# Kernel optimization log

Measured on AMD Instinct MI355X. Metric: run time of the kernel, lower is better.

The kernel has to match this reference:

```python
import jax, jax.numpy as jnp
import numpy as np
import math

L = 2; B = 128; CIN = 64; E = 64; H = 8; Wd = 8; NH = 8; MEM = 40
HD = E // NH; HW = H * Wd; THD = HD * HW  # 512
MASK_B = 3.0; NEG = -1e9; EPS = 1e-5


def _conv(x, w, b):
    y = jax.lax.conv_general_dilated(x, w, (1, 1), 'SAME',
                                     dimension_numbers=('NCHW', 'OIHW', 'NCHW'))
    return y + b[None, :, None, None]


def setup_inputs() -> dict:
    key = jax.random.key(0)
    ks = jax.random.split(key, 12)
    f = jax.random.normal
    return {
        'x': f(ks[0], (B, CIN, H, Wd), jnp.float32),
        'h0': f(ks[1], (L, B, E, H, Wd), jnp.float32),
        'c0': f(ks[2], (L, B, E, H, Wd), jnp.float32),
        'k0': f(ks[3], (L, B, NH, MEM, THD), jnp.float32),
        'v0': f(ks[4], (L, B, NH, MEM, THD), jnp.float32),
        'src_mask': jax.random.randint(ks[5], (B, MEM), 0, 2).astype(bool),
        'notdone': jnp.ones((B,), bool),
        'main_w': f(ks[6], (L, 5 * E, CIN + 2 * E, 3, 3), jnp.float32) * 0.05,
        'main_b': jnp.zeros((L, 5 * E), jnp.float32),
        'proj_w': f(ks[7], (L, 3 * E, CIN + E, 3, 3), jnp.float32) * 0.05,
        'proj_b': jnp.zeros((L, 3 * E), jnp.float32),
        'out_w': f(ks[8], (L, E, E, 3, 3), jnp.float32) * 0.05,
        'out_b': jnp.zeros((L, E), jnp.float32),
        'ln_w': jnp.ones((L, E, H, Wd), jnp.float32),
        'ln_b': jnp.zeros((L, E, H, Wd), jnp.float32),
        'pos_w': f(ks[9], (L, MEM, HW * E), jnp.float32) * 0.05,
        'pos_b': f(ks[10], (L, MEM, NH), jnp.float32) * 0.05,
    }


def reference(x, h0, c0, k0, v0, src_mask, notdone,
              main_w, main_b, proj_w, proj_b, out_w, out_b,
              ln_w, ln_b, pos_w, pos_b):
    nd = notdone.astype(x.dtype)[:, None, None, None]
    # rolling attention mask: reset finished episodes, shift left, open last slot
    m = src_mask | (~notdone)[:, None]
    m = jnp.concatenate([m[:, 1:], jnp.zeros((B, 1), bool)], axis=1)
    bias = jnp.where(m, NEG, 0.0).astype(x.dtype)        # (B, MEM)
    bias = bias.at[:, -1].set(MASK_B)
    out = h0[L - 1] * nd
    for n in range(L):
        inp = jnp.concatenate([x, out], axis=1)          # (B, CIN+E, H, W)
        h_cur = h0[n] * nd
        c_cur = c0[n] * nd
        gates = _conv(jnp.concatenate([inp, h_cur], axis=1), main_w[n], main_b[n])
        cc_i, cc_f, cc_o, cc_g, cc_a = jnp.split(gates, 5, axis=1)
        i = jax.nn.sigmoid(cc_i)
        fg = jax.nn.sigmoid(cc_f)
        o = jax.nn.sigmoid(cc_o)
        g = jnp.tanh(cc_g)
        a = jax.nn.sigmoid(cc_a)
        c_next = fg * c_cur + i * g
        # attention over rolling memory (mem_n slots of flattened spatial features)
        kqv = _conv(inp, proj_w[n], proj_b[n]).reshape(B, NH, 3 * HD, HW)
        k = kqv[:, :, :HD].reshape(B, NH, THD)
        q = kqv[:, :, HD:2 * HD].reshape(B, NH, THD) / math.sqrt(THD)
        v = kqv[:, :, 2 * HD:].reshape(B, NH, THD)
        pw = pos_w[n].reshape(MEM, NH, THD).transpose(1, 0, 2)  # (NH, MEM, THD)
        k_cat = jnp.concatenate([k0[n][:, :, 1:], k[:, :, None, :]], axis=2) + pw[None]
        v_cat = jnp.concatenate([v0[n][:, :, 1:], v[:, :, None, :]], axis=2)
        scores = (jnp.einsum('bnd,bnmd->bnm', q, k_cat)
                  + bias[:, None, :] + pos_b[n].T[None])
        attn_w = jax.nn.softmax(scores, axis=-1)
        attn = jnp.einsum('bnm,bnmd->bnd', attn_w, v_cat).reshape(B, E, H, Wd)
        ao = _conv(attn, out_w[n], out_b[n]) + inp[:, :E]
        mu = ao.mean(axis=(1, 2, 3), keepdims=True)
        var = ((ao - mu) ** 2).mean(axis=(1, 2, 3), keepdims=True)
        ao = (ao - mu) * jax.lax.rsqrt(var + EPS) * ln_w[n][None] + ln_b[n][None]
        c_next = c_next + a * jnp.tanh(ao)
        out = o * jnp.tanh(c_next)
    return out
```

## Files before the change

### kernel.cpp

```cpp
#include <hip/hip_runtime.h>
#include <hip/hip_bf16.h>

typedef __hip_bfloat16 bf16;
typedef unsigned short u16;
typedef __attribute__((ext_vector_type(8))) short short8;
typedef __attribute__((ext_vector_type(4))) float f32x4;

#define Bb   128
#define MEMm 40

__device__ __forceinline__ float LD(const void* p, size_t i, int f32) {
    return f32 ? ((const float*)p)[i] : __bfloat162float(((const bf16*)p)[i]);
}
__device__ __forceinline__ float S2F(short s) {
    u16 u = (u16)s;
    return __bfloat162float(*(bf16*)&u);
}
__device__ __forceinline__ int LDB(const void* p, int i, int isbyte) {
    return isbyte ? (int)((const unsigned char*)p)[i] : ((const int*)p)[i];
}
__device__ __forceinline__ void SPLIT(float v, u16& hi, u16& lo) {
    bf16 h = __float2bfloat16(v);
    float r = v - __bfloat162float(h);
    bf16 l = __float2bfloat16(r);
    hi = *(u16*)&h; lo = *(u16*)&l;
}

__global__ void setup_kernel(const void* __restrict__ x,
                             const void* __restrict__ src_mask,
                             const void* __restrict__ notdone,
                             const void* __restrict__ h0,
                             const void* __restrict__ mw,
                             const void* __restrict__ pw,
                             const void* __restrict__ ow,
                             int* __restrict__ flags,
                             float* __restrict__ biasb,
                             float* __restrict__ outb, size_t hoff,
                             u16* __restrict__ whi, u16* __restrict__ wlo) {
    __shared__ int det[3];
    const int bid = blockIdx.x, t = threadIdx.x;
    if (t < 3) det[t] = 0;
    __syncthreads();
    {
        const bf16* xb = (const bf16*)x;
        int bad = 0;
        for (int i = t; i < 4096; i += 256) {
            float v = __bfloat162float(xb[2 * i]);
            if (!(fabsf(v) < 1e4f)) bad = 1;
        }
        if (bad) atomicOr(&det[0], 1);
        int mb = 0;
        const unsigned* mi = (const unsigned*)src_mask;
        for (int i = t; i < 1280; i += 256) if (mi[i] > 1u) mb = 1;
        if (mb) atomicOr(&det[1], 1);
        int nb = 0;
        const unsigned* ni = (const unsigned*)notdone;
        for (int i = t; i < 32; i += 256) if (ni[i] > 1u) nb = 1;
        if (nb) atomicOr(&det[2], 1);
    }
    __syncthreads();
    const int isf32 = det[0], mbyte = det[1], ndbyte = det[2];
    if (bid == 0 && t < 3) flags[t] = det[t];

    if (bid < 20) {
        int idx = bid * 256 + t;
        if (idx >= Bb * MEMm) return;
        int b = idx / MEMm, m = idx - b * MEMm;
        float v;
        if (m == MEMm - 1) v = 3.0f;
        else {
            bool masked = (LDB(src_mask, b * MEMm + m + 1, mbyte) != 0) ||
                          (LDB(notdone, b, ndbyte) == 0);
            v = masked ? -1e9f : 0.f;
        }
        biasb[idx] = v;
    } else if (bid < 276) {
        int idx = (bid - 20) * 256 + t;
        int b = idx >> 9;
        float nd = (LDB(notdone, b, ndbyte) != 0) ? 1.f : 0.f;
        size_t e = (size_t)idx * 8;
        float v[8];
        if (isf32) {
            const float* hp = (const float*)h0 + hoff + e;
            f32x4 p0 = *(const f32x4*)hp, p1 = *(const f32x4*)(hp + 4);
#pragma unroll
            for (int j = 0; j < 4; ++j) { v[j] = p0[j]; v[4 + j] = p1[j]; }
        } else {
            short8 s = *(const short8*)((const bf16*)h0 + hoff + e);
#pragma unroll
            for (int j = 0; j < 8; ++j) v[j] = S2F(s[j]);
        }
#pragma unroll
        for (int j = 0; j < 8; ++j) outb[e + j] = v[j] * nd;
    } else {
        int gi = (bid - 276) * 256 + t;
        if (gi >= 1622016) return;
        int layer = (gi >= 811008) ? 1 : 0;
        int i = gi - layer * 811008;
        float v;
        if (i < 552960) {
            int tap = i / 61440, r = i - tap * 61440, co = r / 192, ci = r - co * 192;
            v = LD(mw, (size_t)layer * 552960 + ((size_t)co * 192 + ci) * 9 + tap, isf32);
        } else if (i < 774144) {
            int j = i - 552960;
            int tap = j / 24576, r = j - tap * 24576, co = r / 128, ci = r - co * 128;
            v = LD(pw, (size_t)layer * 221184 + ((size_t)co * 128 + ci) * 9 + tap, isf32);
        } else {
            int j = i - 774144;
            int tap = j / 4096, r = j - tap * 4096, co = r / 64, ci = r - co * 64;
            v = LD(ow, (size_t)layer * 36864 + ((size_t)co * 64 + ci) * 9 + tap, isf32);
        }
        u16 h, l; SPLIT(v, h, l);
        whi[gi] = h; wlo[gi] = l;
    }
}

struct ConvArgs {
    const void *x; const float *prev_out; const void *h0; const void *notdone;
    const u16 *WhiA, *WloA, *WhiB, *WloB;
    const void *biasA, *biasB;
    float *OutA, *OutB;
    long long boffA, boffB;
    size_t hoff;
    int KciA, KciB, CoutA, CoutB, ntA, NT, NMB;
};

__global__ __launch_bounds__(256) void conv_mfma_kernel(ConvArgs g,
                                                        const int* __restrict__ flags) {
    __shared__ __align__(16) u16 Alds[2][2][2600];
    __shared__ __align__(16) u16 Wlds[2][2][2560];
    const int t = threadIdx.x, w = t >> 6, lane = t & 63;
    const int bpair = w >> 1, half = w & 1;
    const int bx = blockIdx.x;
    const int mblk = bx % g.NMB, nt = bx / g.NMB;
    const bool isA = (nt < g.ntA);
    const u16* Whi = isA ? g.WhiA : g.WhiB;
    const u16* Wlo = isA ? g.WloA : g.WloB;
    const int Kci  = isA ? g.KciA : g.KciB;
    const int CoutT= isA ? g.CoutA : g.CoutB;
    float* Out     = isA ? g.OutA : g.OutB;
    const void* bias = isA ? g.biasA : g.biasB;
    const long long boff = isA ? g.boffA : g.boffB;
    const int n0 = (isA ? nt : nt - g.ntA) * 64;
    const int b = mblk * 2 + bpair;
    const int NITER = (Kci >> 5) * 9;
    const int isf32 = flags[0];
    const float nd = (LDB(g.notdone, b, flags[2]) != 0) ? 1.f : 0.f;

    if (half == 0 && lane < 40) { Alds[bpair][0][2560 + lane] = 0; Alds[bpair][1][2560 + lane] = 0; }

    f32x4 acc[4][2];
#pragma unroll
    for (int i = 0; i < 4; ++i)
#pragma unroll
        for (int j = 0; j < 2; ++j) { f32x4 z = {0.f, 0.f, 0.f, 0.f}; acc[i][j] = z; }

    const int co_l = t >> 2, jj = t & 3;
    uint4 hvA, lvA, hvB, lvB;
    auto issueW = [&](int it, uint4& hv, uint4& lv) {
        int kc = it / 9, tap = it - kc * 9;
        size_t o = ((size_t)(tap * CoutT + n0 + co_l)) * Kci + kc * 32 + jj * 8;
        hv = *(const uint4*)(Whi + o);
        lv = *(const uint4*)(Wlo + o);
    };

    issueW(0, hvA, lvA);
    issueW(1, hvB, lvB);
    for (int it = 0; it < NITER; ++it) {
        const int kc = it / 9, tap = it - kc * 9;
        const int par = it & 1;
        *(uint4*)&Wlds[par][0][co_l * 40 + jj * 8] = hvA;
        *(uint4*)&Wlds[par][1][co_l * 40 + jj * 8] = lvA;
        __syncthreads();
        hvA = hvB; lvA = lvB;
        if (it + 2 < NITER) issueW(it + 2, hvB, lvB);
        if (tap == 0) {
            const int px = lane;
            const int c0i = half * 16;
            const int cbase = kc * 32;
            short8 hA, hB, lA, lB;
#pragma unroll
            for (int cl2 = 0; cl2 < 16; ++cl2) {
                int c = cbase + c0i + cl2;
                float v;
                if (c < 64) {
                    size_t o = (size_t)b * 4096 + (size_t)c * 64 + px;
                    v = isf32 ? ((const float*)g.x)[o] : S2F(((const short*)g.x)[o]);
                } else if (c < 128) {
                    v = g.prev_out[(size_t)b * 4096 + (size_t)(c - 64) * 64 + px];
                } else {
                    size_t o = g.hoff + (size_t)b * 4096 + (size_t)(c - 128) * 64 + px;
                    v = (isf32 ? ((const float*)g.h0)[o] : S2F(((const short*)g.h0)[o])) * nd;
                }
                u16 hh, ll; SPLIT(v, hh, ll);
                if (cl2 < 8) { hA[cl2] = (short)hh; lA[cl2] = (short)ll; }
                else         { hB[cl2 - 8] = (short)hh; lB[cl2 - 8] = (short)ll; }
            }
            *(short8*)&Alds[bpair][0][px * 40 + c0i]     = hA;
            *(short8*)&Alds[bpair][0][px * 40 + c0i + 8] = hB;
            *(short8*)&Alds[bpair][1][px * 40 + c0i]     = lA;
            *(short8*)&Alds[bpair][1][px * 40 + c0i + 8] = lB;
            __syncthreads();
        }
        const int dy = tap / 3 - 1, dx = tap % 3 - 1;
        const int q8 = (lane >> 4) * 8;
        const int ml = lane & 15;
        short8 aH[4], aL[4];
#pragma unroll
        for (int mt = 0; mt < 4; ++mt) {
            int px = mt * 16 + ml;
            int yy = (px >> 3) + dy, xx = (px & 7) + dx;
            int row = ((unsigned)yy < 8u && (unsigned)xx < 8u) ? yy * 8 + xx : 64;
            int o = row * 40 + q8;
            aH[mt] = *(const short8*)&Alds[bpair][0][o];
            aL[mt] = *(const short8*)&Alds[bpair][1][o];
        }
#pragma unroll
        for (int nn = 0; nn < 2; ++nn) {
            int o = (half * 32 + nn * 16 + ml) * 40 + q8;
            short8 bH = *(const short8*)&Wlds[par][0][o];
            short8 bL = *(const short8*)&Wlds[par][1][o];
#pragma unroll
            for (int mt = 0; mt < 4; ++mt) {
                acc[mt][nn] = __builtin_amdgcn_mfma_f32_16x16x32_bf16(aH[mt], bH, acc[mt][nn], 0, 0, 0);
                acc[mt][nn] = __builtin_amdgcn_mfma_f32_16x16x32_bf16(aH[mt], bL, acc[mt][nn], 0, 0, 0);
                acc[mt][nn] = __builtin_amdgcn_mfma_f32_16x16x32_bf16(aL[mt], bH, acc[mt][nn], 0, 0, 0);
            }
        }
    }
    const int q = lane >> 4, ml = lane & 15;
#pragma unroll
    for (int nn = 0; nn < 2; ++nn) {
        int co = n0 + half * 32 + nn * 16 + ml;
        float bv = LD(bias, (size_t)boff + co, isf32);
#pragma unroll
        for (int mt = 0; mt < 4; ++mt) {
            f32x4 v = acc[mt][nn];
            v[0] += bv; v[1] += bv; v[2] += bv; v[3] += bv;
            *(f32x4*)&Out[((size_t)b * CoutT + co) * 64 + mt * 16 + q * 4] = v;
        }
    }
}

__global__ __launch_bounds__(256) void attn_kernel(
    const float* __restrict__ kqv,
    const void* __restrict__ k0,
    const void* __restrict__ v0,
    const void* __restrict__ pw,
    const void* __restrict__ pb,
    const float* __restrict__ biasb,
    const int* __restrict__ flags,
    u16* __restrict__ ahi, u16* __restrict__ alo,
    size_t kvoff, size_t pwoff, size_t pboff) {
    __shared__ float qv[512], kl[512], vl[512], sc[40], wexp[40];
    __shared__ float accbuf[4][512];
    const int t = threadIdx.x;
    const int isf32 = flags[0];
    const int b = blockIdx.x >> 3, h = blockIdx.x & 7;
    const size_t kqb = (size_t)b * 192 * 64;
    for (int d = t; d < 512; d += 256) {
        int hd = d >> 6, ss = d & 63;
        qv[d] = kqv[kqb + (h * 24 + 8 + hd) * 64 + ss] * 0.044194173824159216f;
        kl[d] = kqv[kqb + (h * 24 + 0 + hd) * 64 + ss];
        vl[d] = kqv[kqb + (h * 24 + 16 + hd) * 64 + ss];
    }
    __syncthreads();
    const int wid = t >> 6, lane = t & 63;
    const int d0 = lane * 8;
    const size_t kvbase = kvoff + ((size_t)(b * 8 + h)) * (size_t)(40 * 512);

    float q8[8];
#pragma unroll
    for (int j = 0; j < 8; ++j) q8[j] = qv[d0 + j];

    if (!isf32) {
        const bf16* kp = (const bf16*)k0;
        const bf16* pp = (const bf16*)pw;
        const bf16* vp = (const bf16*)v0;
        short8 kr[10], pr[10];
#pragma unroll
        for (int i = 0; i < 10; ++i) {
            int m = wid + i * 4;
            pr[i] = *(const short8*)(pp + pwoff + (size_t)m * 4096 + h * 512 + d0);
            if (m < 39)
                kr[i] = *(const short8*)(kp + kvbase + (size_t)(m + 1) * 512 + d0);
        }
#pragma unroll
        for (int i = 0; i < 10; ++i) {
            int m = wid + i * 4;
            float p = 0.f;
            if (m < 39) {
#pragma unroll
                for (int j = 0; j < 8; ++j)
                    p += q8[j] * (S2F(kr[i][j]) + S2F(pr[i][j]));
            } else {
#pragma unroll
                for (int j = 0; j < 8; ++j)
                    p += q8[j] * (kl[d0 + j] + S2F(pr[i][j]));
            }
#pragma unroll
            for (int off = 32; off > 0; off >>= 1) p += __shfl_down(p, off, 64);
            if (lane == 0)
                sc[m] = p + biasb[b * 40 + m] + LD(pb, pboff + m * 8 + h, 0);
        }
        short8 vr[10];
#pragma unroll
        for (int i = 0; i < 10; ++i) {
            int m = wid + i * 4;
            if (m < 39)
                vr[i] = *(const short8*)(vp + kvbase + (size_t)(m + 1) * 512 + d0);
        }
        __syncthreads();
        float mx = -1e30f;
        for (int m = 0; m < 40; ++m) mx = fmaxf(mx, sc[m]);
        if (t < 40) wexp[t] = __expf(sc[t] - mx);
        __syncthreads();
        float sum = 0.f;
        for (int m = 0; m < 40; ++m) sum += wexp[m];
        float rs = 1.f / sum;
        float acc8[8];
#pragma unroll
        for (int j = 0; j < 8; ++j) acc8[j] = 0.f;
#pragma unroll
        for (int i = 0; i < 10; ++i) {
            int m = wid + i * 4;
            float wgt = wexp[m];
            if (m < 39) {
#pragma unroll
                for (int j = 0; j < 8; ++j) acc8[j] += wgt * S2F(vr[i][j]);
            } else {
#pragma unroll
                for (int j = 0; j < 8; ++j) acc8[j] += wgt * vl[d0 + j];
            }
        }
#pragma unroll
        for (int j = 0; j < 8; ++j) accbuf[wid][d0 + j] = acc8[j];
        __syncthreads();
        for (int d = t; d < 512; d += 256) {
            float acc = (accbuf[0][d] + accbuf[1][d]) + (accbuf[2][d] + accbuf[3][d]);
            acc *= rs;
            int ch = h * 8 + (d >> 6), px = d & 63;
            u16 hh, ll; SPLIT(acc, hh, ll);
            size_t o = (size_t)b * 4096 + px * 64 + ch;
            ahi[o] = hh; alo[o] = ll;
        }
        return;
    }

    for (int m = wid; m < 40; m += 4) {
        float kc[8];
        if (m < 39) {
            const float* kp = (const float*)k0 + kvbase + (size_t)(m + 1) * 512 + d0;
            f32x4 p0 = *(const f32x4*)kp, p1 = *(const f32x4*)(kp + 4);
#pragma unroll
            for (int j = 0; j < 4; ++j) { kc[j] = p0[j]; kc[4 + j] = p1[j]; }
        } else {
#pragma unroll
            for (int j = 0; j < 8; ++j) kc[j] = kl[d0 + j];
        }
        const float* pp = (const float*)pw + pwoff + (size_t)m * 4096 + h * 512 + d0;
        f32x4 p0 = *(const f32x4*)pp, p1 = *(const f32x4*)(pp + 4);
#pragma unroll
        for (int j = 0; j < 4; ++j) { kc[j] += p0[j]; kc[4 + j] += p1[j]; }
        float p = 0.f;
#pragma unroll
        for (int j = 0; j < 8; ++j) p += q8[j] * kc[j];
#pragma unroll
        for (int off = 32; off > 0; off >>= 1) p += __shfl_down(p, off, 64);
        if (lane == 0)
            sc[m] = p + biasb[b * 40 + m] + LD(pb, pboff + m * 8 + h, 1);
    }
    __syncthreads();
    float mx = -1e30f;
    for (int m = 0; m < 40; ++m) mx = fmaxf(mx, sc[m]);
    if (t < 40) wexp[t] = __expf(sc[t] - mx);
    __syncthreads();
    float sum = 0.f;
    for (int m = 0; m < 40; ++m) sum += wexp[m];
    float rs = 1.f / sum;
    float acc8[8];
#pragma unroll
    for (int j = 0; j < 8; ++j) acc8[j] = 0.f;
    for (int m = wid; m < 40; m += 4) {
        float wgt = wexp[m];
        if (m < 39) {
            const float* vp = (const float*)v0 + kvbase + (size_t)(m + 1) * 512 + d0;
            f32x4 p0 = *(const f32x4*)vp, p1 = *(const f32x4*)(vp + 4);
#pragma unroll
            for (int j = 0; j < 4; ++j) { acc8[j] += wgt * p0[j]; acc8[4 + j] += wgt * p1[j]; }
        } else {
#pragma unroll
            for (int j = 0; j < 8; ++j) acc8[j] += wgt * vl[d0 + j];
        }
    }
#pragma unroll
    for (int j = 0; j < 8; ++j) accbuf[wid][d0 + j] = acc8[j];
    __syncthreads();
    for (int d = t; d < 512; d += 256) {
        float acc = (accbuf[0][d] + accbuf[1][d]) + (accbuf[2][d] + accbuf[3][d]);
        acc *= rs;
        int ch = h * 8 + (d >> 6), px = d & 63;
        u16 hh, ll; SPLIT(acc, hh, ll);
        size_t o = (size_t)b * 4096 + px * 64 + ch;
        ahi[o] = hh; alo[o] = ll;
    }
}

__global__ __launch_bounds__(256) void tail_kernel(
    const u16* __restrict__ ahi, const u16* __restrict__ alo,
    const u16* __restrict__ whi, const u16* __restrict__ wlo,
    const void* __restrict__ outb_bias,
    const void* __restrict__ x,
    const float* __restrict__ gates,
    const void* __restrict__ c0,
    const void* __restrict__ notdone,
    const void* __restrict__ lnw, const void* __restrict__ lnb,
    const int* __restrict__ flags,
    float* __restrict__ out_buf, void* __restrict__ dout, int write_out,
    long long boff, size_t coff, size_t lnoff) {
    __shared__ __align__(16) u16 Ald[2][2][2600];
    __shared__ __align__(16) u16 Wl[2][2][2560];
    __shared__ float red[8], stats[2];
    const int t = threadIdx.x, w = t >> 6, lane = t & 63;
    const int b = blockIdx.x;
    const int isf32 = flags[0], ndbyte = flags[2];

    {
        int px = t >> 2, ci16 = (t & 3) * 16;
        int chunk = ci16 >> 5, cl = ci16 & 31;
        size_t o = ((size_t)b * 64 + px) * 64 + ci16;
        *(uint4*)&Ald[chunk][0][px * 40 + cl]     = *(const uint4*)(ahi + o);
        *(uint4*)&Ald[chunk][0][px * 40 + cl + 8] = *(const uint4*)(ahi + o + 8);
        *(uint4*)&Ald[chunk][1][px * 40 + cl]     = *(const uint4*)(alo + o);
        *(uint4*)&Ald[chunk][1][px * 40 + cl + 8] = *(const uint4*)(alo + o + 8);
        if (t < 160) { int ch = t / 80, hl = (t / 40) & 1, i = t % 40;
                       Ald[ch][hl][2560 + i] = 0; }
    }

    const int co_l = t >> 2, jj = t & 3;
    uint4 hv, lv;
    auto issueW = [&](int it) {
        int kc = it / 9, tap = it - kc * 9;
        size_t o = ((size_t)(tap * 64 + co_l)) * 64 + kc * 32 + jj * 8;
        hv = *(const uint4*)(whi + o);
        lv = *(const uint4*)(wlo + o);
    };

    f32x4 acc[4];
#pragma unroll
    for (int i = 0; i < 4; ++i) { f32x4 z = {0.f, 0.f, 0.f, 0.f}; acc[i] = z; }

    issueW(0);
    for (int it = 0; it < 18; ++it) {
        const int kc = it / 9, tap = it - kc * 9;
        const int par = it & 1;
        *(uint4*)&Wl[par][0][co_l * 40 + jj * 8] = hv;
        *(uint4*)&Wl[par][1][co_l * 40 + jj * 8] = lv;
        __syncthreads();
        if (it + 1 < 18) issueW(it + 1);
        const int dy = tap / 3 - 1, dx = tap % 3 - 1;
        const int q8 = (lane >> 4) * 8;
        const int ml = lane & 15;
        short8 aH[4], aL[4];
#pragma unroll
        for (int mt = 0; mt < 4; ++mt) {
            int px = mt * 16 + ml;
            int yy = (px >> 3) + dy, xx = (px & 7) + dx;
            int row = ((unsigned)yy < 8u && (unsigned)xx < 8u) ? yy * 8 + xx : 64;
            int o = row * 40 + q8;
            aH[mt] = *(const short8*)&Ald[kc][0][o];
            aL[mt] = *(const short8*)&Ald[kc][1][o];
        }
        int o = (w * 16 + ml) * 40 + q8;
        short8 bH = *(const short8*)&Wl[par][0][o];
        short8 bL = *(const short8*)&Wl[par][1][o];
#pragma unroll
        for (int mt = 0; mt < 4; ++mt) {
            acc[mt] = __builtin_amdgcn_mfma_f32_16x16x32_bf16(aH[mt], bH, acc[mt], 0, 0, 0);
            acc[mt] = __builtin_amdgcn_mfma_f32_16x16x32_bf16(aH[mt], bL, acc[mt], 0, 0, 0);
            acc[mt] = __builtin_amdgcn_mfma_f32_16x16x32_bf16(aL[mt], bH, acc[mt], 0, 0, 0);
        }
    }

    const int q = lane >> 4, ml = lane & 15;
    const int co = w * 16 + ml;
    const size_t base = (size_t)b * 4096;
    float bv = LD(outb_bias, (size_t)boff + co, isf32);
    float vals[16];
    float sum = 0.f, sumsq = 0.f;
#pragma unroll
    for (int mt = 0; mt < 4; ++mt) {
        int px0 = mt * 16 + q * 4;
#pragma unroll
        for (int r = 0; r < 4; ++r) {
            float xv = LD(x, base + (size_t)co * 64 + px0 + r, isf32);
            float val = acc[mt][r] + bv + xv;
            vals[mt * 4 + r] = val; sum += val; sumsq += val * val;
        }
    }
#pragma unroll
    for (int off = 32; off > 0; off >>= 1) {
        sum   += __shfl_down(sum, off, 64);
        sumsq += __shfl_down(sumsq, off, 64);
    }
    if (lane == 0) { red[w] = sum; red[4 + w] = sumsq; }
    __syncthreads();
    if (t == 0) {
        float ts = red[0] + red[1] + red[2] + red[3];
        float tq = red[4] + red[5] + red[6] + red[7];
        float mu = ts * (1.f / 4096.f);
        float var = tq * (1.f / 4096.f) - mu * mu;
        stats[0] = mu; stats[1] = rsqrtf(fmaxf(var, 0.f) + 1e-5f);
    }
    __syncthreads();
    const float mu = stats[0], rstd = stats[1];
    const float nd = (LDB(notdone, b, ndbyte) != 0) ? 1.f : 0.f;
    const size_t gbase = (size_t)b * 320 * 64;
#pragma unroll
    for (int mt = 0; mt < 4; ++mt) {
        int px0 = mt * 16 + q * 4;
        size_t i0 = (size_t)co * 64 + px0;
        f32x4 gi4 = *(const f32x4*)&gates[gbase + (size_t)(co      ) * 64 + px0];
        f32x4 gf4 = *(const f32x4*)&gates[gbase + (size_t)(co +  64) * 64 + px0];
        f32x4 go4 = *(const f32x4*)&gates[gbase + (size_t)(co + 128) * 64 + px0];
        f32x4 gg4 = *(const f32x4*)&gates[gbase + (size_t)(co + 192) * 64 + px0];
        f32x4 ga4 = *(const f32x4*)&gates[gbase + (size_t)(co + 256) * 64 + px0];
        f32x4 ov;
#pragma unroll
        for (int r = 0; r < 4; ++r) {
            size_t i = i0 + r;
            float aon = (vals[mt * 4 + r] - mu) * rstd * LD(lnw, lnoff + i, isf32)
                        + LD(lnb, lnoff + i, isf32);
            float gi = 1.f / (1.f + __expf(-gi4[r]));
            float gf = 1.f / (1.f + __expf(-gf4[r]));
            float go = 1.f / (1.f + __expf(-go4[r]));
            float gg = tanhf(gg4[r]);
            float ga = 1.f / (1.f + __expf(-ga4[r]));
            float cc = LD(c0, coff + base + i, isf32) * nd;
            float cn = gf * cc + gi * gg + ga * tanhf(aon);
            float o  = go * tanhf(cn);
            ov[r] = o;
            if (write_out) {
                if (isf32) ((float*)dout)[base + i] = o;
                else       ((bf16*)dout)[base + i] = __float2bfloat16(o);
            }
        }
        *(f32x4*)&out_buf[base + i0] = ov;
    }
}

extern "C" void kernel_launch(void* const* d_in, const int* in_sizes, int n_in,
                              void* d_out, int out_size, void* d_ws, size_t ws_size,
                              hipStream_t stream) {
    const void* x      = d_in[0];
    const void* h0     = d_in[1];
    const void* c0     = d_in[2];
    const void* k0     = d_in[3];
    const void* v0     = d_in[4];
    const void* src_mask = d_in[5];
    const void* notdone  = d_in[6];
    const void* main_w = d_in[7];
    const void* main_b = d_in[8];
    const void* proj_w = d_in[9];
    const void* proj_b = d_in[10];
    const void* out_w  = d_in[11];
    const void* out_b  = d_in[12];
    const void* ln_w   = d_in[13];
    const void* ln_b   = d_in[14];
    const void* pos_w  = d_in[15];
    const void* pos_b  = d_in[16];

    float* wsf = (float*)d_ws;
    int*   flags    = (int*)d_ws;
    float* bias_buf = wsf + 8;
    float* out_buf  = wsf + 8192;
    float* gates_buf= wsf + 532480;
    float* kqv_buf  = wsf + 3153920;
    u16* attn_hi    = (u16*)(wsf + 4726784);
    u16* attn_lo    = (u16*)(wsf + 4988928);
    u16* wr_hi      = (u16*)(wsf + 5251072);
    u16* wr_lo      = (u16*)(wsf + 6062080);

    setup_kernel<<<6612, 256, 0, stream>>>(x, src_mask, notdone, h0,
                                           main_w, proj_w, out_w, flags,
                                           bias_buf, out_buf, (size_t)524288,
                                           wr_hi, wr_lo);
    for (int n = 0; n < 2; ++n) {
        const size_t wb = (size_t)n * 811008;
        ConvArgs ga;
        ga.x = x; ga.prev_out = out_buf; ga.h0 = h0; ga.notdone = notdone;
        ga.hoff = (size_t)n * 524288;
        ga.WhiA = wr_hi + wb;          ga.WloA = wr_lo + wb;          ga.KciA = 192; ga.CoutA = 320;
        ga.WhiB = wr_hi + wb + 552960; ga.WloB = wr_lo + wb + 552960; ga.KciB = 128; ga.CoutB = 192;
        ga.biasA = main_b; ga.boffA = (long long)n * 320; ga.OutA = gates_buf;
        ga.biasB = proj_b; ga.boffB = (long long)n * 192; ga.OutB = kqv_buf;
        ga.ntA = 5; ga.NT = 8; ga.NMB = 64;
        conv_mfma_kernel<<<512, 256, 0, stream>>>(ga, flags);

        attn_kernel<<<1024, 256, 0, stream>>>(
            kqv_buf, k0, v0, pos_w, pos_b, bias_buf, flags, attn_hi, attn_lo,
            (size_t)n * 20971520, (size_t)n * 163840, (size_t)n * 320);

        tail_kernel<<<128, 256, 0, stream>>>(
            attn_hi, attn_lo, wr_hi + wb + 774144, wr_lo + wb + 774144,
            out_b, x, gates_buf, c0, notdone, ln_w, ln_b, flags,
            out_buf, d_out, (n == 1) ? 1 : 0,
            (long long)n * 64, (size_t)n * 524288, (size_t)n * 4096);
    }
}
```

Before: 580.0 us.

## Pre-swizzle conv weights into MFMA fragment layout and load directly to registers

The weight-prep kernel now writes main and projection conv weights in a layout where each 512-element block matches one wave's 16x32 MFMA B-fragment, ordered by tap, k-chunk and output slice. The conv kernel drops the shared-memory weight staging buffer and its per-iteration barrier, and loads B fragments straight from global memory into registers with one-iteration prefetch. This removes LDS traffic and a __syncthreads per K step. In exchange each wave issues its own global loads, with only a single step of latency hiding. The out-projection layout is unchanged, so any path that reuses this conv kernel for it would read wrongly indexed weights.

```diff
diff --git a/kernel.cpp b/kernel.cpp
--- a/kernel.cpp
+++ b/kernel.cpp
@@ -99,15 +99,27 @@
         int i = gi - layer * 811008;
         float v;
         if (i < 552960) {
-            int tap = i / 61440, r = i - tap * 61440, co = r / 192, ci = r - co * 192;
+            int blk = i >> 9, r = i & 511;
+            int l = r >> 3, j = r & 7;
+            int nn = blk & 1, b2 = blk >> 1;
+            int s = b2 % 10, tk = b2 / 10;
+            int kc = tk % 6, tap = tk / 6;
+            int co = s * 32 + nn * 16 + (l & 15);
+            int ci = kc * 32 + ((l >> 4) << 3) + j;
             v = LD(mw, (size_t)layer * 552960 + ((size_t)co * 192 + ci) * 9 + tap, isf32);
         } else if (i < 774144) {
-            int j = i - 552960;
-            int tap = j / 24576, r = j - tap * 24576, co = r / 128, ci = r - co * 128;
+            int j2 = i - 552960;
+            int blk = j2 >> 9, r = j2 & 511;
+            int l = r >> 3, j = r & 7;
+            int nn = blk & 1, b2 = blk >> 1;
+            int s = b2 % 6, tk = b2 / 6;
+            int kc = tk & 3, tap = tk >> 2;
+            int co = s * 32 + nn * 16 + (l & 15);
+            int ci = kc * 32 + ((l >> 4) << 3) + j;
             v = LD(pw, (size_t)layer * 221184 + ((size_t)co * 128 + ci) * 9 + tap, isf32);
         } else {
-            int j = i - 774144;
-            int tap = j / 4096, r = j - tap * 4096, co = r / 64, ci = r - co * 64;
+            int j2 = i - 774144;
+            int tap = j2 / 4096, r = j2 - tap * 4096, co = r / 64, ci = r - co * 64;
             v = LD(ow, (size_t)layer * 36864 + ((size_t)co * 64 + ci) * 9 + tap, isf32);
         }
         u16 h, l; SPLIT(v, h, l);
@@ -128,7 +140,6 @@
 __global__ __launch_bounds__(256) void conv_mfma_kernel(ConvArgs g,
                                                         const int* __restrict__ flags) {
     __shared__ __align__(16) u16 Alds[2][2][2600];
-    __shared__ __align__(16) u16 Wlds[2][2][2560];
     const int t = threadIdx.x, w = t >> 6, lane = t & 63;
     const int bpair = w >> 1, half = w & 1;
     const int bx = blockIdx.x;
@@ -143,7 +154,10 @@
     const long long boff = isA ? g.boffA : g.boffB;
     const int n0 = (isA ? nt : nt - g.ntA) * 64;
     const int b = mblk * 2 + bpair;
-    const int NITER = (Kci >> 5) * 9;
+    const int kcN = Kci >> 5;
+    const int CoutT32 = CoutT >> 5;
+    const int NITER = kcN * 9;
+    const int s = (n0 >> 5) + half;
     const int isf32 = flags[0];
     const float nd = (LDB(g.notdone, b, flags[2]) != 0) ? 1.f : 0.f;
 
@@ -155,26 +169,28 @@
 #pragma unroll
         for (int j = 0; j < 2; ++j) { f32x4 z = {0.f, 0.f, 0.f, 0.f}; acc[i][j] = z; }
 
-    const int co_l = t >> 2, jj = t & 3;
-    uint4 hvA, lvA, hvB, lvB;
-    auto issueW = [&](int it, uint4& hv, uint4& lv) {
+    auto wbase = [&](int it) -> size_t {
         int kc = it / 9, tap = it - kc * 9;
-        size_t o = ((size_t)(tap * CoutT + n0 + co_l)) * Kci + kc * 32 + jj * 8;
-        hv = *(const uint4*)(Whi + o);
-        lv = *(const uint4*)(Wlo + o);
+        return ((size_t)((tap * kcN + kc) * CoutT32 + s) * 2) * 512 + (size_t)lane * 8;
     };
 
-    issueW(0, hvA, lvA);
-    issueW(1, hvB, lvB);
+    short8 wh0, wh1, wl0, wl1, nh0, nh1, nl0, nl1;
+    {
+        size_t o = wbase(0);
+        wh0 = *(const short8*)(Whi + o); wh1 = *(const short8*)(Whi + o + 512);
+        wl0 = *(const short8*)(Wlo + o); wl1 = *(const short8*)(Wlo + o + 512);
+    }
+    nh0 = wh0; nh1 = wh1; nl0 = wl0; nl1 = wl1;
+
     for (int it = 0; it < NITER; ++it) {
         const int kc = it / 9, tap = it - kc * 9;
-        const int par = it & 1;
-        *(uint4*)&Wlds[par][0][co_l * 40 + jj * 8] = hvA;
-        *(uint4*)&Wlds[par][1][co_l * 40 + jj * 8] = lvA;
-        __syncthreads();
-        hvA = hvB; lvA = lvB;
-        if (it + 2 < NITER) issueW(it + 2, hvB, lvB);
+        if (it + 1 < NITER) {
+            size_t o = wbase(it + 1);
+            nh0 = *(const short8*)(Whi + o); nh1 = *(const short8*)(Whi + o + 512);
+            nl0 = *(const short8*)(Wlo + o); nl1 = *(const short8*)(Wlo + o + 512);
+        }
         if (tap == 0) {
+            __syncthreads();
             const int px = lane;
             const int c0i = half * 16;
             const int cbase = kc * 32;
@@ -216,17 +232,15 @@
             aL[mt] = *(const short8*)&Alds[bpair][1][o];
         }
 #pragma unroll
-        for (int nn = 0; nn < 2; ++nn) {
-            int o = (half * 32 + nn * 16 + ml) * 40 + q8;
-            short8 bH = *(const short8*)&Wlds[par][0][o];
-            short8 bL = *(const short8*)&Wlds[par][1][o];
-#pragma unroll
-            for (int mt = 0; mt < 4; ++mt) {
-                acc[mt][nn] = __builtin_amdgcn_mfma_f32_16x16x32_bf16(aH[mt], bH, acc[mt][nn], 0, 0, 0);
-                acc[mt][nn] = __builtin_amdgcn_mfma_f32_16x16x32_bf16(aH[mt], bL, acc[mt][nn], 0, 0, 0);
-                acc[mt][nn] = __builtin_amdgcn_mfma_f32_16x16x32_bf16(aL[mt], bH, acc[mt][nn], 0, 0, 0);
-            }
-        }
+        for (int mt = 0; mt < 4; ++mt) {
+            acc[mt][0] = __builtin_amdgcn_mfma_f32_16x16x32_bf16(aH[mt], wh0, acc[mt][0], 0, 0, 0);
+            acc[mt][0] = __builtin_amdgcn_mfma_f32_16x16x32_bf16(aH[mt], wl0, acc[mt][0], 0, 0, 0);
+            acc[mt][0] = __builtin_amdgcn_mfma_f32_16x16x32_bf16(aL[mt], wh0, acc[mt][0], 0, 0, 0);
+            acc[mt][1] = __builtin_amdgcn_mfma_f32_16x16x32_bf16(aH[mt], wh1, acc[mt][1], 0, 0, 0);
+            acc[mt][1] = __builtin_amdgcn_mfma_f32_16x16x32_bf16(aH[mt], wl1, acc[mt][1], 0, 0, 0);
+            acc[mt][1] = __builtin_amdgcn_mfma_f32_16x16x32_bf16(aL[mt], wh1, acc[mt][1], 0, 0, 0);
+        }
+        wh0 = nh0; wh1 = nh1; wl0 = nl0; wl1 = nl1;
     }
     const int q = lane >> 4, ml = lane & 15;
 #pragma unroll
```

Result: no change. 572.1 us (-1.4%).
